# Kernel optimization log

Measured on AMD Instinct MI355X. Metric: run time of the kernel, lower is better.

## Reference

```python
import jax, jax.numpy as jnp
import numpy as np

M0 = 0.3
R = 2
H = W = 64  # grid size from init_kwargs
N = H * W
B = 2


def _make_grid():
    # grid_by(lims=[[1,-1],[-1,1]], size=(64,64)): cartesian_prod of the two
    # linspaces, then columns swapped via index_select([1, 0]).
    a = jnp.linspace(1.0, -1.0, H)
    b = jnp.linspace(-1.0, 1.0, W)
    ga, gb = jnp.meshgrid(a, b, indexing='ij')
    cart = jnp.stack([ga, gb], axis=-1).reshape(N, 2)  # cartesian_prod order
    return cart[:, ::-1]  # swap columns -> [N, 2]


def setup_inputs() -> dict:
    key = jax.random.key(0)
    k1, k2 = jax.random.split(key)
    grid = _make_grid()
    # input points = grid + small jitter (avoids exactly-zero distances)
    inp = grid[None, :, :] + 0.05 * jax.random.normal(k1, (B, N, 2), dtype=jnp.float32)
    weight = jax.random.uniform(k2, (B, N), dtype=jnp.float32)
    return {"input": inp, "weight": weight, "grid": grid}


def reference(input, weight, grid):
    # --- brute-force KNN (r=2), k = N (full sort; equivalent to torch max_k path) ---
    # dist[b, j, i] = || grid_j - input_{b,i} ||_2   (note the .mT in torch knn)
    d2 = jnp.sum((grid[None, :, None, :] - input[:, None, :, :]) ** 2, axis=-1)  # [B,N,N]
    dist = jnp.sqrt(d2)
    order = jnp.argsort(dist, axis=-1)                       # ascending distance
    knn_dist = jnp.take_along_axis(dist, order, axis=-1)     # [B,N,N]
    knn_index = order                                        # indices into input points

    # --- weighted DTM ---
    weight_bound = M0 * jnp.sum(weight, axis=-1, keepdims=True)   # [B,1]
    wb = weight_bound[:, :, None]                                  # [B,1,1]
    # gather per-row weights of the sorted neighbors
    knn_weight = jax.vmap(lambda w, idx: w[idx])(weight, knn_index)  # [B,N,N]
    cum_knn_weight = jnp.cumsum(knn_weight, axis=-1)
    # searchsorted (left): first index where cumulative weight >= bound
    k_index = jnp.sum(cum_knn_weight < wb, axis=-1, keepdims=True)   # [B,N,1]
    k_index = jnp.minimum(k_index, N - 1)

    r_dist = knn_dist ** 2  # r == 2
    cum_dist = jnp.cumsum(r_dist * knn_weight, axis=-1)
    dtm_val = jnp.take_along_axis(
        cum_dist + r_dist * (wb - cum_knn_weight), k_index, axis=-1
    ).squeeze(-1)                                                    # [B,N]
    return jnp.sqrt(dtm_val / weight_bound)
```

## Files before the change

### kernel.cpp

```cpp
#include <hip/hip_runtime.h>
#include <math.h>

namespace {

constexpr int   kN       = 4096;
constexpr int   kThreads = 256;
constexpr int   kEPT     = kN / 64;
constexpr int   kGroups  = kEPT / 2;
constexpr int   kIters   = 9;
constexpr float kM0      = 0.3f;
constexpr float kS       = 2048.f;
constexpr float kRootS   = 45.25483399593904f;

typedef _Float16 h2 __attribute__((ext_vector_type(2)));

__device__ __forceinline__ float waveReduceSum(float v) {
#pragma unroll
    for (int off = 32; off >= 1; off >>= 1) v += __shfl_xor(v, off);
    return v;
}

__device__ __forceinline__ void waveReduceSum2(float& x, float& y) {
#pragma unroll
    for (int off = 32; off >= 1; off >>= 1) {
        const float xs = __shfl_xor(x, off);
        const float ys = __shfl_xor(y, off);
        x += xs;
        y += ys;
    }
}

__device__ __forceinline__ h2 clamp01(h2 t, h2 zero2, h2 one2) {
    return __builtin_elementwise_min(__builtin_elementwise_max(t, zero2), one2);
}

__global__ __launch_bounds__(kThreads)
void dtm_kernel(const float* __restrict__ input,
                const float* __restrict__ weight,
                const float* __restrict__ grid,
                float* __restrict__ out,
                int nq) {
    const int lane = threadIdx.x & 63;
    const int wave = threadIdx.x >> 6;
    const int wglob = blockIdx.x * 4 + wave;
    const int b    = wglob >> 11;
    const int wid  = wglob & 2047;
    const int i0 = wid;
    const int i1 = wid + kN / 2;
    if (b * kN + i1 >= nq) return;

    const float sgxA = kRootS * grid[2 * i0], sgyA = kRootS * grid[2 * i0 + 1];
    const float sgxB = kRootS * grid[2 * i1], sgyB = kRootS * grid[2 * i1 + 1];
    const float4* inp4 = (const float4*)(input + (size_t)b * kN * 2);
    const float4* wgt4 = (const float4*)(weight + (size_t)b * kN);

    const h2 zero2 = h2{(_Float16)0.f, (_Float16)0.f};
    const h2 one2  = h2{(_Float16)1.f, (_Float16)1.f};

    h2 dA[kGroups], dB[kGroups], ws[kGroups];
    float wl = 0.f;
#pragma unroll
    for (int s = 0; s < kGroups / 2; ++s) {
        const int g = lane + 64 * s;
        const float4 wv = wgt4[g];
        const float4 pa = inp4[2 * g];
        const float4 pb = inp4[2 * g + 1];
        float dx, dy, e0, e1, e2, e3;
        dx = fmaf(-kRootS, pa.x, sgxA); dy = fmaf(-kRootS, pa.y, sgyA); e0 = fmaf(dy, dy, dx * dx);
        dx = fmaf(-kRootS, pa.z, sgxA); dy = fmaf(-kRootS, pa.w, sgyA); e1 = fmaf(dy, dy, dx * dx);
        dx = fmaf(-kRootS, pb.x, sgxA); dy = fmaf(-kRootS, pb.y, sgyA); e2 = fmaf(dy, dy, dx * dx);
        dx = fmaf(-kRootS, pb.z, sgxA); dy = fmaf(-kRootS, pb.w, sgyA); e3 = fmaf(dy, dy, dx * dx);
        dA[2 * s]     = h2{(_Float16)e0, (_Float16)e1};
        dA[2 * s + 1] = h2{(_Float16)e2, (_Float16)e3};
        dx = fmaf(-kRootS, pa.x, sgxB); dy = fmaf(-kRootS, pa.y, sgyB); e0 = fmaf(dy, dy, dx * dx);
        dx = fmaf(-kRootS, pa.z, sgxB); dy = fmaf(-kRootS, pa.w, sgyB); e1 = fmaf(dy, dy, dx * dx);
        dx = fmaf(-kRootS, pb.x, sgxB); dy = fmaf(-kRootS, pb.y, sgyB); e2 = fmaf(dy, dy, dx * dx);
        dx = fmaf(-kRootS, pb.z, sgxB); dy = fmaf(-kRootS, pb.w, sgyB); e3 = fmaf(dy, dy, dx * dx);
        dB[2 * s]     = h2{(_Float16)e0, (_Float16)e1};
        dB[2 * s + 1] = h2{(_Float16)e2, (_Float16)e3};
        ws[2 * s]     = h2{(_Float16)wv.x, (_Float16)wv.y};
        ws[2 * s + 1] = h2{(_Float16)wv.z, (_Float16)wv.w};
        wl = __builtin_amdgcn_fdot2(ws[2 * s],     one2, wl, false);
        wl = __builtin_amdgcn_fdot2(ws[2 * s + 1], one2, wl, false);
    }
    const float wb = kM0 * waveReduceSum(wl);

    float loA = 0.f, hiA = 32768.f, TloA = 0.f;
    float loB = 0.f, hiB = 32768.f, TloB = 0.f;
#pragma unroll
    for (int it = 0; it < kIters; ++it) {
        const float midA = 0.5f * (loA + hiA);
        const float midB = 0.5f * (loB + hiB);
        const _Float16 mAh = (_Float16)midA;
        const _Float16 mBh = (_Float16)midB;
        const h2 mA2 = h2{mAh, mAh};
        const h2 mB2 = h2{mBh, mBh};
        float a0 = 0.f, a1 = 0.f, b0 = 0.f, b1 = 0.f;
#pragma unroll
        for (int g = 0; g < kGroups; g += 2) {
            h2 tA0 = clamp01(mA2 - dA[g],     zero2, one2);
            h2 tA1 = clamp01(mA2 - dA[g + 1], zero2, one2);
            h2 tB0 = clamp01(mB2 - dB[g],     zero2, one2);
            h2 tB1 = clamp01(mB2 - dB[g + 1], zero2, one2);
            a0 = __builtin_amdgcn_fdot2(ws[g],     tA0, a0, false);
            a1 = __builtin_amdgcn_fdot2(ws[g + 1], tA1, a1, false);
            b0 = __builtin_amdgcn_fdot2(ws[g],     tB0, b0, false);
            b1 = __builtin_amdgcn_fdot2(ws[g + 1], tB1, b1, false);
        }
        float TA = a0 + a1, TB = b0 + b1;
        waveReduceSum2(TA, TB);
        if (TA >= wb) hiA = midA; else { loA = midA; TloA = TA; }
        if (TB >= wb) hiB = midB; else { loB = midB; TloB = TB; }
    }

    {
        const _Float16 lAh = (_Float16)loA;
        const _Float16 lBh = (_Float16)loB;
        const h2 lA2 = h2{lAh, lAh};
        const h2 lB2 = h2{lBh, lBh};
        float A0 = 0.f, A1 = 0.f, B0 = 0.f, B1 = 0.f;
#pragma unroll
        for (int g = 0; g < kGroups; g += 2) {
            const h2 tA0 = clamp01(lA2 - dA[g],     zero2, one2);
            const h2 tA1 = clamp01(lA2 - dA[g + 1], zero2, one2);
            const h2 tB0 = clamp01(lB2 - dB[g],     zero2, one2);
            const h2 tB1 = clamp01(lB2 - dB[g + 1], zero2, one2);
            const h2 pA0 = dA[g] * ws[g];
            const h2 pA1 = dA[g + 1] * ws[g + 1];
            const h2 pB0 = dB[g] * ws[g];
            const h2 pB1 = dB[g + 1] * ws[g + 1];
            A0 = __builtin_amdgcn_fdot2(pA0, tA0, A0, false);
            A1 = __builtin_amdgcn_fdot2(pA1, tA1, A1, false);
            B0 = __builtin_amdgcn_fdot2(pB0, tB0, B0, false);
            B1 = __builtin_amdgcn_fdot2(pB1, tB1, B1, false);
        }
        float AA = A0 + A1, AB = B0 + B1;
        waveReduceSum2(AA, AB);
        if (lane == 0) {
            const float dtmA = (AA + hiA * (wb - TloA)) * (1.f / kS);
            const float dtmB = (AB + hiB * (wb - TloB)) * (1.f / kS);
            float* ob = out + (size_t)b * kN;
            ob[i0] = sqrtf(fmaxf(dtmA, 0.f) / wb);
            ob[i1] = sqrtf(fmaxf(dtmB, 0.f) / wb);
        }
    }
}

}

extern "C" void kernel_launch(void* const* d_in, const int* in_sizes, int n_in,
                              void* d_out, int out_size, void* d_ws, size_t ws_size,
                              hipStream_t stream) {
    const float* input  = (const float*)d_in[0];
    const float* weight = (const float*)d_in[1];
    const float* grid   = (const float*)d_in[2];
    float* out = (float*)d_out;
    const int nq = out_size;
    const int blocks = (nq + 7) / 8;
    dtm_kernel<<<dim3(blocks), dim3(kThreads), 0, stream>>>(input, weight, grid, out, nq);
}
```

Before: 76.61 us.

## Process four queries per wave with DPP reductions and fused clamp-subtract

Each wave now handles four query points in two passes instead of two. It keeps the scaled input coordinates and weights in fp16 registers and recomputes the distances in packed fp16 for each pair, so the global loads and weight reduction are shared across more queries. The shuffle-based wave reductions become DPP row operations plus a readlane, and the sub/max/min clamp becomes a single v_pk_add_f16 with the clamp modifier. Computing distances in fp16 rather than fp32 lowers precision, and the grid launch is halved with a launch_bounds occupancy hint.

```diff
diff --git a/kernel.cpp b/kernel.cpp
--- a/kernel.cpp
+++ b/kernel.cpp
@@ -3,38 +3,52 @@
 
 namespace {
 
-constexpr int   kN       = 4096;
+constexpr int   kN      = 4096;
 constexpr int   kThreads = 256;
-constexpr int   kEPT     = kN / 64;
-constexpr int   kGroups  = kEPT / 2;
-constexpr int   kIters   = 9;
-constexpr float kM0      = 0.3f;
-constexpr float kS       = 2048.f;
-constexpr float kRootS   = 45.25483399593904f;
+constexpr int   kIters  = 9;
+constexpr float kM0     = 0.3f;
+constexpr float kS      = 2048.f;
+constexpr float kRootS  = 45.25483399593904f;
 
 typedef _Float16 h2 __attribute__((ext_vector_type(2)));
 
-__device__ __forceinline__ float waveReduceSum(float v) {
-#pragma unroll
-    for (int off = 32; off >= 1; off >>= 1) v += __shfl_xor(v, off);
-    return v;
+__device__ __forceinline__ h2 pkrtz(float a, float b) {
+    return __builtin_bit_cast(h2, __builtin_amdgcn_cvt_pkrtz(a, b));
+}
+__device__ __forceinline__ float rdl63(float x) {
+    return __builtin_bit_cast(float, __builtin_amdgcn_readlane(__builtin_bit_cast(int, x), 63));
+}
+template <int kCtrl, int kRmask>
+__device__ __forceinline__ void dppStep2(float& x, float& y) {
+    const int xi = __builtin_amdgcn_update_dpp(0, __builtin_bit_cast(int, x), kCtrl, kRmask, 0xf, true);
+    const int yi = __builtin_amdgcn_update_dpp(0, __builtin_bit_cast(int, y), kCtrl, kRmask, 0xf, true);
+    x += __builtin_bit_cast(float, xi);
+    y += __builtin_bit_cast(float, yi);
+}
+__device__ __forceinline__ void waveSum2(float& x, float& y) {
+    dppStep2<0x111, 0xf>(x, y);
+    dppStep2<0x112, 0xf>(x, y);
+    dppStep2<0x114, 0xf>(x, y);
+    dppStep2<0x118, 0xf>(x, y);
+    dppStep2<0x142, 0xa>(x, y);
+    dppStep2<0x143, 0xc>(x, y);
+    x = rdl63(x);
+    y = rdl63(y);
+}
+__device__ __forceinline__ float waveSum1(float x) {
+    float y = 0.f;
+    waveSum2(x, y);
+    return x;
 }
 
-__device__ __forceinline__ void waveReduceSum2(float& x, float& y) {
-#pragma unroll
-    for (int off = 32; off >= 1; off >>= 1) {
-        const float xs = __shfl_xor(x, off);
-        const float ys = __shfl_xor(y, off);
-        x += xs;
-        y += ys;
-    }
+__device__ __forceinline__ h2 subClamp01(h2 m, h2 d) {
+    h2 r;
+    asm("v_pk_add_f16 %0, %1, %2 neg_lo:[0,1] neg_hi:[0,1] clamp"
+        : "=v"(r) : "v"(m), "v"(d));
+    return r;
 }
 
-__device__ __forceinline__ h2 clamp01(h2 t, h2 zero2, h2 one2) {
-    return __builtin_elementwise_min(__builtin_elementwise_max(t, zero2), one2);
-}
-
-__global__ __launch_bounds__(kThreads)
+__global__ __launch_bounds__(kThreads, 2)
 void dtm_kernel(const float* __restrict__ input,
                 const float* __restrict__ weight,
                 const float* __restrict__ grid,
@@ -42,106 +56,114 @@
                 int nq) {
     const int lane = threadIdx.x & 63;
     const int wave = threadIdx.x >> 6;
-    const int wglob = blockIdx.x * 4 + wave;
-    const int b    = wglob >> 11;
-    const int wid  = wglob & 2047;
-    const int i0 = wid;
-    const int i1 = wid + kN / 2;
-    if (b * kN + i1 >= nq) return;
+    const int wg   = blockIdx.x * 4 + wave;
+    const int b    = wg >> 10;
+    const int base = wg & 1023;
+    if ((b << 12) >= nq) return;
 
-    const float sgxA = kRootS * grid[2 * i0], sgyA = kRootS * grid[2 * i0 + 1];
-    const float sgxB = kRootS * grid[2 * i1], sgyB = kRootS * grid[2 * i1 + 1];
     const float4* inp4 = (const float4*)(input + (size_t)b * kN * 2);
     const float4* wgt4 = (const float4*)(weight + (size_t)b * kN);
 
-    const h2 zero2 = h2{(_Float16)0.f, (_Float16)0.f};
-    const h2 one2  = h2{(_Float16)1.f, (_Float16)1.f};
+    const h2 one2 = h2{(_Float16)1.f, (_Float16)1.f};
 
-    h2 dA[kGroups], dB[kGroups], ws[kGroups];
-    float wl = 0.f;
+    h2 spx[32], spy[32], ws[32];
+    float wl0 = 0.f, wl1 = 0.f;
 #pragma unroll
-    for (int s = 0; s < kGroups / 2; ++s) {
+    for (int s = 0; s < 16; ++s) {
         const int g = lane + 64 * s;
         const float4 wv = wgt4[g];
         const float4 pa = inp4[2 * g];
         const float4 pb = inp4[2 * g + 1];
-        float dx, dy, e0, e1, e2, e3;
-        dx = fmaf(-kRootS, pa.x, sgxA); dy = fmaf(-kRootS, pa.y, sgyA); e0 = fmaf(dy, dy, dx * dx);
-        dx = fmaf(-kRootS, pa.z, sgxA); dy = fmaf(-kRootS, pa.w, sgyA); e1 = fmaf(dy, dy, dx * dx);
-        dx = fmaf(-kRootS, pb.x, sgxA); dy = fmaf(-kRootS, pb.y, sgyA); e2 = fmaf(dy, dy, dx * dx);
-        dx = fmaf(-kRootS, pb.z, sgxA); dy = fmaf(-kRootS, pb.w, sgyA); e3 = fmaf(dy, dy, dx * dx);
-        dA[2 * s]     = h2{(_Float16)e0, (_Float16)e1};
-        dA[2 * s + 1] = h2{(_Float16)e2, (_Float16)e3};
-        dx = fmaf(-kRootS, pa.x, sgxB); dy = fmaf(-kRootS, pa.y, sgyB); e0 = fmaf(dy, dy, dx * dx);
-        dx = fmaf(-kRootS, pa.z, sgxB); dy = fmaf(-kRootS, pa.w, sgyB); e1 = fmaf(dy, dy, dx * dx);
-        dx = fmaf(-kRootS, pb.x, sgxB); dy = fmaf(-kRootS, pb.y, sgyB); e2 = fmaf(dy, dy, dx * dx);
-        dx = fmaf(-kRootS, pb.z, sgxB); dy = fmaf(-kRootS, pb.w, sgyB); e3 = fmaf(dy, dy, dx * dx);
-        dB[2 * s]     = h2{(_Float16)e0, (_Float16)e1};
-        dB[2 * s + 1] = h2{(_Float16)e2, (_Float16)e3};
-        ws[2 * s]     = h2{(_Float16)wv.x, (_Float16)wv.y};
-        ws[2 * s + 1] = h2{(_Float16)wv.z, (_Float16)wv.w};
-        wl = __builtin_amdgcn_fdot2(ws[2 * s],     one2, wl, false);
-        wl = __builtin_amdgcn_fdot2(ws[2 * s + 1], one2, wl, false);
+        spx[2 * s]     = pkrtz(kRootS * pa.x, kRootS * pa.z);
+        spy[2 * s]     = pkrtz(kRootS * pa.y, kRootS * pa.w);
+        spx[2 * s + 1] = pkrtz(kRootS * pb.x, kRootS * pb.z);
+        spy[2 * s + 1] = pkrtz(kRootS * pb.y, kRootS * pb.w);
+        ws[2 * s]      = pkrtz(wv.x, wv.y);
+        ws[2 * s + 1]  = pkrtz(wv.z, wv.w);
+        wl0 = __builtin_amdgcn_fdot2(ws[2 * s],     one2, wl0, false);
+        wl1 = __builtin_amdgcn_fdot2(ws[2 * s + 1], one2, wl1, false);
     }
-    const float wb = kM0 * waveReduceSum(wl);
+    const float wb = kM0 * waveSum1(wl0 + wl1);
 
-    float loA = 0.f, hiA = 32768.f, TloA = 0.f;
-    float loB = 0.f, hiB = 32768.f, TloB = 0.f;
+    float* ob = out + (size_t)b * kN;
+
 #pragma unroll
-    for (int it = 0; it < kIters; ++it) {
-        const float midA = 0.5f * (loA + hiA);
-        const float midB = 0.5f * (loB + hiB);
-        const _Float16 mAh = (_Float16)midA;
-        const _Float16 mBh = (_Float16)midB;
-        const h2 mA2 = h2{mAh, mAh};
-        const h2 mB2 = h2{mBh, mBh};
-        float a0 = 0.f, a1 = 0.f, b0 = 0.f, b1 = 0.f;
+    for (int p = 0; p < 2; ++p) {
+        const int iA = base + (p << 11);
+        const int iB = iA + 1024;
+        const _Float16 gxA = (_Float16)(kRootS * grid[2 * iA]);
+        const _Float16 gyA = (_Float16)(kRootS * grid[2 * iA + 1]);
+        const _Float16 gxB = (_Float16)(kRootS * grid[2 * iB]);
+        const _Float16 gyB = (_Float16)(kRootS * grid[2 * iB + 1]);
+        const h2 gxA2 = h2{gxA, gxA}, gyA2 = h2{gyA, gyA};
+        const h2 gxB2 = h2{gxB, gxB}, gyB2 = h2{gyB, gyB};
+
+        h2 dA[32], dB[32];
 #pragma unroll
-        for (int g = 0; g < kGroups; g += 2) {
-            h2 tA0 = clamp01(mA2 - dA[g],     zero2, one2);
-            h2 tA1 = clamp01(mA2 - dA[g + 1], zero2, one2);
-            h2 tB0 = clamp01(mB2 - dB[g],     zero2, one2);
-            h2 tB1 = clamp01(mB2 - dB[g + 1], zero2, one2);
-            a0 = __builtin_amdgcn_fdot2(ws[g],     tA0, a0, false);
-            a1 = __builtin_amdgcn_fdot2(ws[g + 1], tA1, a1, false);
-            b0 = __builtin_amdgcn_fdot2(ws[g],     tB0, b0, false);
-            b1 = __builtin_amdgcn_fdot2(ws[g + 1], tB1, b1, false);
+        for (int g = 0; g < 32; ++g) {
+            const h2 ax = gxA2 - spx[g], ay = gyA2 - spy[g];
+            dA[g] = ay * ay + ax * ax;
+            const h2 bx = gxB2 - spx[g], by = gyB2 - spy[g];
+            dB[g] = by * by + bx * bx;
         }
-        float TA = a0 + a1, TB = b0 + b1;
-        waveReduceSum2(TA, TB);
-        if (TA >= wb) hiA = midA; else { loA = midA; TloA = TA; }
-        if (TB >= wb) hiB = midB; else { loB = midB; TloB = TB; }
-    }
 
-    {
-        const _Float16 lAh = (_Float16)loA;
-        const _Float16 lBh = (_Float16)loB;
-        const h2 lA2 = h2{lAh, lAh};
-        const h2 lB2 = h2{lBh, lBh};
-        float A0 = 0.f, A1 = 0.f, B0 = 0.f, B1 = 0.f;
+        float loA = 0.f, hiA = 32768.f, TloA = 0.f;
+        float loB = 0.f, hiB = 32768.f, TloB = 0.f;
 #pragma unroll
-        for (int g = 0; g < kGroups; g += 2) {
-            const h2 tA0 = clamp01(lA2 - dA[g],     zero2, one2);
-            const h2 tA1 = clamp01(lA2 - dA[g + 1], zero2, one2);
-            const h2 tB0 = clamp01(lB2 - dB[g],     zero2, one2);
-            const h2 tB1 = clamp01(lB2 - dB[g + 1], zero2, one2);
-            const h2 pA0 = dA[g] * ws[g];
-            const h2 pA1 = dA[g + 1] * ws[g + 1];
-            const h2 pB0 = dB[g] * ws[g];
-            const h2 pB1 = dB[g + 1] * ws[g + 1];
-            A0 = __builtin_amdgcn_fdot2(pA0, tA0, A0, false);
-            A1 = __builtin_amdgcn_fdot2(pA1, tA1, A1, false);
-            B0 = __builtin_amdgcn_fdot2(pB0, tB0, B0, false);
-            B1 = __builtin_amdgcn_fdot2(pB1, tB1, B1, false);
+        for (int it = 0; it < kIters; ++it) {
+            const float midA = 0.5f * (loA + hiA);
+            const float midB = 0.5f * (loB + hiB);
+            const _Float16 mAh = (_Float16)midA;
+            const _Float16 mBh = (_Float16)midB;
+            const h2 mA2 = h2{mAh, mAh};
+            const h2 mB2 = h2{mBh, mBh};
+            float a0 = 0.f, a1 = 0.f, b0 = 0.f, b1 = 0.f;
+#pragma unroll
+            for (int g = 0; g < 32; g += 2) {
+                const h2 tA0 = subClamp01(mA2, dA[g]);
+                const h2 tA1 = subClamp01(mA2, dA[g + 1]);
+                const h2 tB0 = subClamp01(mB2, dB[g]);
+                const h2 tB1 = subClamp01(mB2, dB[g + 1]);
+                a0 = __builtin_amdgcn_fdot2(ws[g],     tA0, a0, false);
+                a1 = __builtin_amdgcn_fdot2(ws[g + 1], tA1, a1, false);
+                b0 = __builtin_amdgcn_fdot2(ws[g],     tB0, b0, false);
+                b1 = __builtin_amdgcn_fdot2(ws[g + 1], tB1, b1, false);
+            }
+            float TA = a0 + a1, TB = b0 + b1;
+            waveSum2(TA, TB);
+            if (TA >= wb) hiA = midA; else { loA = midA; TloA = TA; }
+            if (TB >= wb) hiB = midB; else { loB = midB; TloB = TB; }
         }
-        float AA = A0 + A1, AB = B0 + B1;
-        waveReduceSum2(AA, AB);
-        if (lane == 0) {
-            const float dtmA = (AA + hiA * (wb - TloA)) * (1.f / kS);
-            const float dtmB = (AB + hiB * (wb - TloB)) * (1.f / kS);
-            float* ob = out + (size_t)b * kN;
-            ob[i0] = sqrtf(fmaxf(dtmA, 0.f) / wb);
-            ob[i1] = sqrtf(fmaxf(dtmB, 0.f) / wb);
+
+        {
+            const _Float16 lAh = (_Float16)loA;
+            const _Float16 lBh = (_Float16)loB;
+            const h2 lA2 = h2{lAh, lAh};
+            const h2 lB2 = h2{lBh, lBh};
+            float A0 = 0.f, A1 = 0.f, B0 = 0.f, B1 = 0.f;
+#pragma unroll
+            for (int g = 0; g < 32; g += 2) {
+                const h2 tA0 = subClamp01(lA2, dA[g]);
+                const h2 tA1 = subClamp01(lA2, dA[g + 1]);
+                const h2 tB0 = subClamp01(lB2, dB[g]);
+                const h2 tB1 = subClamp01(lB2, dB[g + 1]);
+                const h2 pA0 = dA[g] * ws[g];
+                const h2 pA1 = dA[g + 1] * ws[g + 1];
+                const h2 pB0 = dB[g] * ws[g];
+                const h2 pB1 = dB[g + 1] * ws[g + 1];
+                A0 = __builtin_amdgcn_fdot2(pA0, tA0, A0, false);
+                A1 = __builtin_amdgcn_fdot2(pA1, tA1, A1, false);
+                B0 = __builtin_amdgcn_fdot2(pB0, tB0, B0, false);
+                B1 = __builtin_amdgcn_fdot2(pB1, tB1, B1, false);
+            }
+            float AA = A0 + A1, AB = B0 + B1;
+            waveSum2(AA, AB);
+            if (lane == 0) {
+                const float dtmA = (AA + hiA * (wb - TloA)) * (1.f / kS);
+                const float dtmB = (AB + hiB * (wb - TloB)) * (1.f / kS);
+                ob[iA] = sqrtf(fmaxf(dtmA, 0.f) / wb);
+                ob[iB] = sqrtf(fmaxf(dtmB, 0.f) / wb);
+            }
         }
     }
 }
@@ -156,6 +178,6 @@
     const float* grid   = (const float*)d_in[2];
     float* out = (float*)d_out;
     const int nq = out_size;
-    const int blocks = (nq + 7) / 8;
+    const int blocks = (nq + 15) / 16;
     dtm_kernel<<<dim3(blocks), dim3(kThreads), 0, stream>>>(input, weight, grid, out, nq);
 }
```

Result: no change. 76.60 us (-0.0%).
